# Performance work log

Hardware: AMD Instinct MI355X
Metric: run time of the kernel (lower is better)

The kernel has to match this reference:

```python
import jax, jax.numpy as jnp
import numpy as np

H = 16
D_MODEL = 1024
D_K = D_MODEL // H


def setup_inputs() -> dict:
    key = jax.random.key(0)
    ks = jax.random.split(key, 11)
    B, S = 2, 2048
    scale = 1.0 / np.sqrt(D_MODEL)
    inp = {
        "query": jax.random.normal(ks[0], (B, S, D_MODEL), dtype=jnp.float32),
        "key": jax.random.normal(ks[1], (B, S, D_MODEL), dtype=jnp.float32),
        "value": jax.random.normal(ks[2], (B, S, D_MODEL), dtype=jnp.float32),
        "Wq": jax.random.normal(ks[3], (D_MODEL, D_MODEL), dtype=jnp.float32) * scale,
        "bq": jnp.zeros((D_MODEL,), dtype=jnp.float32),
        "Wk": jax.random.normal(ks[4], (D_MODEL, D_MODEL), dtype=jnp.float32) * scale,
        "bk": jnp.zeros((D_MODEL,), dtype=jnp.float32),
        "Wv": jax.random.normal(ks[5], (D_MODEL, D_MODEL), dtype=jnp.float32) * scale,
        "bv": jnp.zeros((D_MODEL,), dtype=jnp.float32),
        "Wo": jax.random.normal(ks[6], (D_MODEL, D_MODEL), dtype=jnp.float32) * scale,
        "bo": jnp.zeros((D_MODEL,), dtype=jnp.float32),
    }
    return inp


def _mha(query, key, value, Wq, bq, Wk, bk, Wv, bv, Wo, bo):
    B, S, _ = query.shape
    # linear projections (torch nn.Linear: x @ W.T + b)
    q = query @ Wq.T + bq
    k = key @ Wk.T + bk
    v = value @ Wv.T + bv
    # split heads: [B, S, D] -> [B, H, S, d_k]
    q = q.reshape(B, S, H, D_K).transpose(0, 2, 1, 3)
    k = k.reshape(B, S, H, D_K).transpose(0, 2, 1, 3)
    v = v.reshape(B, S, H, D_K).transpose(0, 2, 1, 3)
    # scaled dot-product attention with manual stable softmax
    scores = jnp.einsum("bhqd,bhkd->bhqk", q, k) / jnp.sqrt(jnp.float32(D_K))
    stable = scores - jnp.max(scores, axis=-1, keepdims=True)
    e = jnp.exp(stable)
    attn = e / jnp.sum(e, axis=-1, keepdims=True)
    ctx = jnp.einsum("bhqk,bhkd->bhqd", attn, v)
    # merge heads and final projection
    ctx = ctx.transpose(0, 2, 1, 3).reshape(B, S, H * D_K)
    return ctx @ Wo.T + bo


def reference(query, key, value, Wq, bq, Wk, bk, Wv, bv, Wo, bo):
    return _mha(query, key, value, Wq, bq, Wk, bk, Wv, bv, Wo, bo)
```

## Files before the change

kernel.cpp:

```cpp
#include <hip/hip_runtime.h>


#define S_LEN 2048
#define BATCH 2
#define DM    1024
#define NH    16
#define DKH   64
#define BS    (BATCH * S_LEN)

typedef _Float16 f16x8 __attribute__((ext_vector_type(8)));
typedef _Float16 f16x4 __attribute__((ext_vector_type(4)));
typedef _Float16 f16x2 __attribute__((ext_vector_type(2)));
typedef __fp16   h16x2 __attribute__((ext_vector_type(2)));
typedef float    f32x4 __attribute__((ext_vector_type(4)));
typedef float    f32x16 __attribute__((ext_vector_type(16)));

__device__ __forceinline__ f16x2 pk_f16(float a, float b) {
  h16x2 r = __builtin_amdgcn_cvt_pkrtz(a, b);
  return __builtin_bit_cast(f16x2, r);
}

__device__ __forceinline__ void gld16(const void* g, void* l) {
  __builtin_amdgcn_global_load_lds(
      (const __attribute__((address_space(1))) void*)g,
      (__attribute__((address_space(3))) void*)l, 16, 0, 0);
}

__device__ __forceinline__ float fast_exp2(float x) {
#if __has_builtin(__builtin_amdgcn_exp2f)
  return __builtin_amdgcn_exp2f(x);
#else
  return exp2f(x);
#endif
}

__device__ __forceinline__ int swap23(int x) {
  return (x & ~12) | ((x & 4) << 1) | ((x & 8) >> 1);
}

__device__ __forceinline__ f16x8 cvt8(const float* __restrict__ p) {
  float4 x0 = *(const float4*)p;
  float4 x1 = *(const float4*)(p + 4);
  f16x2 c0 = pk_f16(x0.x, x0.y), c1 = pk_f16(x0.z, x0.w);
  f16x2 c2 = pk_f16(x1.x, x1.y), c3 = pk_f16(x1.z, x1.w);
  f16x8 h;
  h[0] = c0[0]; h[1] = c0[1]; h[2] = c1[0]; h[3] = c1[1];
  h[4] = c2[0]; h[5] = c2[1]; h[6] = c3[0]; h[7] = c3[1];
  return h;
}

template <typename OUT_T, bool VT, bool A32, bool B32>
__device__ __forceinline__ void gemm_core(
    const void* __restrict__ Av, const void* __restrict__ Wv,
    const float* __restrict__ bias, OUT_T* __restrict__ out, float oscale)
{
  const int tid  = threadIdx.x;
  const int l    = tid & 63;
  const int wv   = tid >> 6;
  const int c    = l & 15, quad = l >> 4;
  const int m0   = blockIdx.x * 128, n0 = blockIdx.y * 128;
  const int wm   = wv & 1, wn = wv >> 1;
  __shared__ _Float16 sA[128 * 64];
  __shared__ _Float16 sB[128 * 64];

  const _Float16* gA16[4]; const float* gA32[4];
  const _Float16* gB16[4]; const float* gB32[4];
#pragma unroll
  for (int p = 0; p < 4; ++p) {
    int s = tid + p * 256, r = s >> 3, g = (s & 7) ^ (r & 7);
    if constexpr (A32) gA32[p] = (const float*)Av + (size_t)(m0 + r) * DM + g * 8;
    else               gA16[p] = (const _Float16*)Av + (size_t)(m0 + r) * DM + g * 8;
    if constexpr (B32) gB32[p] = (const float*)Wv + (size_t)(n0 + r) * DM + g * 8;
    else               gB16[p] = (const _Float16*)Wv + (size_t)(n0 + r) * DM + g * 8;
  }
  const int cx = c & 7;

  f32x4 acc[4][4] = {};
  for (int k0 = 0; k0 < DM; k0 += 64) {
    __syncthreads();
    if constexpr (!A32) {
#pragma unroll
      for (int p = 0; p < 4; ++p) gld16(gA16[p] + k0, sA + (tid + p * 256) * 8);
    }
    if constexpr (!B32) {
#pragma unroll
      for (int p = 0; p < 4; ++p) gld16(gB16[p] + k0, sB + (tid + p * 256) * 8);
    }
    if constexpr (A32) {
      f16x8 st[4];
#pragma unroll
      for (int p = 0; p < 4; ++p) st[p] = cvt8(gA32[p] + k0);
#pragma unroll
      for (int p = 0; p < 4; ++p) *(f16x8*)(sA + (tid + p * 256) * 8) = st[p];
    }
    if constexpr (B32) {
      f16x8 st[4];
#pragma unroll
      for (int p = 0; p < 4; ++p) st[p] = cvt8(gB32[p] + k0);
#pragma unroll
      for (int p = 0; p < 4; ++p) *(f16x8*)(sB + (tid + p * 256) * 8) = st[p];
    }
    __syncthreads();
#pragma unroll
    for (int ks = 0; ks < 2; ++ks) {
      f16x8 af[4], bf[4];
#pragma unroll
      for (int i = 0; i < 4; ++i)
        af[i] = *(const f16x8*)&sA[(wm * 64 + i * 16 + c) * 64 + ((ks * 4 + quad) ^ cx) * 8];
#pragma unroll
      for (int j = 0; j < 4; ++j)
        bf[j] = *(const f16x8*)&sB[(wn * 64 + j * 16 + c) * 64 + ((ks * 4 + quad) ^ cx) * 8];
#pragma unroll
      for (int i = 0; i < 4; ++i)
#pragma unroll
        for (int j = 0; j < 4; ++j) {
          if constexpr (VT)
            acc[i][j] = __builtin_amdgcn_mfma_f32_16x16x32_f16(af[i], bf[j], acc[i][j], 0, 0, 0);
          else
            acc[j][i] = __builtin_amdgcn_mfma_f32_16x16x32_f16(bf[j], af[i], acc[j][i], 0, 0, 0);
        }
    }
  }
  if constexpr (VT) {
#pragma unroll
    for (int j = 0; j < 4; ++j) {
      int col = n0 + wn * 64 + j * 16 + c;
      float bb = bias[col];
      int hh = col >> 6, dd = col & 63;
#pragma unroll
      for (int i = 0; i < 4; ++i) {
        int row = m0 + wm * 64 + i * 16 + quad * 4;
        int bb2 = row >> 11, ss = row & (S_LEN - 1);
        _Float16* dst = (_Float16*)out + ((size_t)(bb2 * NH + hh) * DKH + dd) * S_LEN + ss;
        f16x4 v4;
#pragma unroll
        for (int r = 0; r < 4; ++r) v4[r] = (_Float16)((acc[i][j][r] + bb) * oscale);
        *(f16x4*)dst = v4;
      }
    }
  } else {
#pragma unroll
    for (int j = 0; j < 4; ++j) {
      const int nb = n0 + wn * 64 + j * 16 + quad * 4;
      const f32x4 bb = *(const f32x4*)(bias + nb);
#pragma unroll
      for (int i = 0; i < 4; ++i) {
        const int m = m0 + wm * 64 + i * 16 + c;
        if constexpr (__is_same(OUT_T, float)) {
          f32x4 v4;
#pragma unroll
          for (int r = 0; r < 4; ++r) v4[r] = (acc[j][i][r] + bb[r]) * oscale;
          *(f32x4*)((float*)out + (size_t)m * DM + nb) = v4;
        } else {
          f16x4 v4;
#pragma unroll
          for (int r = 0; r < 4; ++r) v4[r] = (_Float16)((acc[j][i][r] + bb[r]) * oscale);
          *(f16x4*)((_Float16*)out + (size_t)m * DM + nb) = v4;
        }
      }
    }
  }
}

#define SC_Q (0.125f * 1.44269504088896340736f)

__global__ __launch_bounds__(256) void proj3(
    const float* __restrict__ xq, const float* __restrict__ xk, const float* __restrict__ xv,
    const float* __restrict__ wqp, const float* __restrict__ wkp, const float* __restrict__ wvp,
    const float* __restrict__ bq, const float* __restrict__ bk, const float* __restrict__ bv,
    _Float16* __restrict__ Q, _Float16* __restrict__ K, _Float16* __restrict__ Vt)
{
  const int z = blockIdx.z;
  if (z == 2) {
    gemm_core<_Float16, true, true, true>(xv, wvp, bv, Vt, 1.0f);
  } else if (z == 0) {
    gemm_core<_Float16, false, true, true>(xq, wqp, bq, Q, SC_Q);
  } else {
    gemm_core<_Float16, false, true, true>(xk, wkp, bk, K, 1.0f);
  }
}

__global__ __launch_bounds__(256) void out_gemm(
    const _Float16* __restrict__ ctx, const float* __restrict__ wo,
    const float* __restrict__ bo, float* __restrict__ out)
{
  gemm_core<float, false, false, true>(ctx, wo, bo, out, 1.0f);
}

__global__ __launch_bounds__(256, 2) void attn(
    const _Float16* __restrict__ Q, const _Float16* __restrict__ K,
    const _Float16* __restrict__ Vt, _Float16* __restrict__ ctx)
{
  const int tid = threadIdx.x;
  const int l   = tid & 63, wv = tid >> 6;
  const int lo5 = l & 31, hf = l >> 5;
  const int wq  = wv >> 1, wk = wv & 1;
  const int bh  = blockIdx.x;
  const int q0  = blockIdx.y * 128;
  const int b   = bh >> 4, hd = bh & 15;
  __shared__ _Float16 sK[2][64 * 64];
  __shared__ _Float16 sV[2][64 * 64];

  f16x8 qf0[4], qf1[4];
  {
    const _Float16* Qg0 = Q + ((size_t)(b * S_LEN + q0 + wq * 64 + lo5)) * DM + hd * DKH + 8 * hf;
    const _Float16* Qg1 = Qg0 + (size_t)32 * DM;
#pragma unroll
    for (int kc = 0; kc < 4; ++kc) { qf0[kc] = *(const f16x8*)(Qg0 + 16 * kc);
                                     qf1[kc] = *(const f16x8*)(Qg1 + 16 * kc); }
  }

  f32x16 o0[2] = {}, o1[2] = {};
  float l0 = 0.f, l1 = 0.f;
  const f16x2 ones = {(_Float16)1.0f, (_Float16)1.0f};

  const _Float16* Kg0 = K + ((size_t)b * S_LEN) * DM + hd * DKH;
  const _Float16* Vg0 = Vt + ((size_t)bh * DKH) * S_LEN;

  const int sa = tid,       ra = sa >> 3, ba = (sa & 7) ^ (ra & 7);
  const int sb = tid + 256, rb = sb >> 3, bb = (sb & 7) ^ (rb & 7);
  const _Float16* gKa = Kg0 + (size_t)swap23(ra) * DM + ba * 8;
  const _Float16* gKb = Kg0 + (size_t)swap23(rb) * DM + bb * 8;
  const _Float16* gVa = Vg0 + (size_t)ra * S_LEN + ba * 8;
  const _Float16* gVb = Vg0 + (size_t)rb * S_LEN + bb * 8;
  const int rx = lo5 & 7;

#define STAGE(t, bf) do {                                   \
    const size_t k0s = (size_t)(t) * 64;                    \
    gld16(gKa + k0s * DM, sK[bf] + sa * 8);                 \
    gld16(gKb + k0s * DM, sK[bf] + sb * 8);                 \
    gld16(gVa + k0s,      sV[bf] + sa * 8);                 \
    gld16(gVb + k0s,      sV[bf] + sb * 8);                 \
  } while (0)

  STAGE(0, 0);
  asm volatile("s_waitcnt vmcnt(0)" ::: "memory");
  __builtin_amdgcn_s_barrier();

  const int NT = S_LEN / 64;
  for (int kt = 0; kt < NT; ++kt) {
    const int cur = kt & 1;
    if (kt + 1 < NT) STAGE(kt + 1, cur ^ 1);

    const _Float16* sKc = sK[cur];
    const _Float16* sVc = sV[cur];

    f32x16 sA0 = {}, sA1 = {};
    __builtin_amdgcn_s_setprio(1);
#pragma unroll
    for (int kc = 0; kc < 4; ++kc) {
      f16x8 kf = *(const f16x8*)&sKc[(32 * wk + lo5) * 64 + ((2 * kc + hf) ^ rx) * 8];
      sA0 = __builtin_amdgcn_mfma_f32_32x32x16_f16(kf, qf0[kc], sA0, 0, 0, 0);
      sA1 = __builtin_amdgcn_mfma_f32_32x32x16_f16(kf, qf1[kc], sA1, 0, 0, 0);
    }
    __builtin_amdgcn_s_setprio(0);

    f16x8 p0[2], p1[2];
#pragma unroll
    for (int half = 0; half < 2; ++half)
#pragma unroll
      for (int j2 = 0; j2 < 4; ++j2) {
        float a0 = fast_exp2(sA0[8 * half + 2 * j2]);
        float a1 = fast_exp2(sA0[8 * half + 2 * j2 + 1]);
        f16x2 pka = pk_f16(a0, a1);
        p0[half][2 * j2]     = pka[0];
        p0[half][2 * j2 + 1] = pka[1];
        l0 = __builtin_amdgcn_fdot2(__builtin_bit_cast(h16x2, pka),
                                    __builtin_bit_cast(h16x2, ones), l0, false);
        float b0 = fast_exp2(sA1[8 * half + 2 * j2]);
        float b1 = fast_exp2(sA1[8 * half + 2 * j2 + 1]);
        f16x2 pkb = pk_f16(b0, b1);
        p1[half][2 * j2]     = pkb[0];
        p1[half][2 * j2 + 1] = pkb[1];
        l1 = __builtin_amdgcn_fdot2(__builtin_bit_cast(h16x2, pkb),
                                    __builtin_bit_cast(h16x2, ones), l1, false);
      }

    __builtin_amdgcn_s_setprio(1);
#pragma unroll
    for (int db = 0; db < 2; ++db)
#pragma unroll
      for (int half = 0; half < 2; ++half) {
        const int kc2 = 2 * wk + half;
        f16x8 vf = *(const f16x8*)&sVc[(32 * db + lo5) * 64 + ((2 * kc2 + hf) ^ rx) * 8];
        o0[db] = __builtin_amdgcn_mfma_f32_32x32x16_f16(p0[half], vf, o0[db], 0, 0, 0);
        o1[db] = __builtin_amdgcn_mfma_f32_32x32x16_f16(p1[half], vf, o1[db], 0, 0, 0);
      }
    __builtin_amdgcn_s_setprio(0);

    if (kt + 1 < NT) {
      asm volatile("s_waitcnt vmcnt(0)" ::: "memory");
      __builtin_amdgcn_s_barrier();
    }
  }
#undef STAGE

  __syncthreads();

  l0 += __shfl_xor(l0, 32);
  l1 += __shfl_xor(l1, 32);
  float* lbuf = (float*)&sV[0][0];
  float* obuf = (float*)&sK[0][0];
  if (hf == 0) {
    lbuf[((wq * 2 + 0) * 2 + wk) * 32 + lo5] = l0;
    lbuf[((wq * 2 + 1) * 2 + wk) * 32 + lo5] = l1;
  }
  __syncthreads();

  float inv0[16], inv1[16];
#pragma unroll
  for (int r = 0; r < 16; ++r) {
    int qq = 8 * (r >> 2) + 4 * hf + (r & 3);
    inv0[r] = 1.0f / (lbuf[((wq * 2 + 0) * 2 + 0) * 32 + qq] +
                      lbuf[((wq * 2 + 0) * 2 + 1) * 32 + qq]);
    inv1[r] = 1.0f / (lbuf[((wq * 2 + 1) * 2 + 0) * 32 + qq] +
                      lbuf[((wq * 2 + 1) * 2 + 1) * 32 + qq]);
  }

  _Float16* Og = ctx + ((size_t)(b * S_LEN + q0 + wq * 64)) * DM + hd * DKH;
#pragma unroll
  for (int db = 0; db < 2; ++db) {
    if (wk == 1) {
#pragma unroll
      for (int r = 0; r < 16; ++r) {
        int qq = 8 * (r >> 2) + 4 * hf + (r & 3);
        obuf[((wq * 2 + 0) * 32 + qq) * 32 + lo5] = o0[db][r];
        obuf[((wq * 2 + 1) * 32 + qq) * 32 + lo5] = o1[db][r];
      }
    }
    __syncthreads();
    if (wk == 0) {
#pragma unroll
      for (int r = 0; r < 16; ++r) {
        int qq = 8 * (r >> 2) + 4 * hf + (r & 3);
        float v0 = o0[db][r] + obuf[((wq * 2 + 0) * 32 + qq) * 32 + lo5];
        float v1 = o1[db][r] + obuf[((wq * 2 + 1) * 32 + qq) * 32 + lo5];
        Og[(size_t)qq * DM + 32 * db + lo5]        = (_Float16)(v0 * inv0[r]);
        Og[(size_t)(32 + qq) * DM + 32 * db + lo5] = (_Float16)(v1 * inv1[r]);
      }
    }
    __syncthreads();
  }
}

extern "C" void kernel_launch(void* const* d_in, const int* in_sizes, int n_in,
                              void* d_out, int out_size, void* d_ws, size_t ws_size,
                              hipStream_t stream)
{
  (void)in_sizes; (void)n_in; (void)out_size; (void)ws_size;
  const float* q  = (const float*)d_in[0];
  const float* k  = (const float*)d_in[1];
  const float* v  = (const float*)d_in[2];
  const float* wq = (const float*)d_in[3];
  const float* bq = (const float*)d_in[4];
  const float* wk = (const float*)d_in[5];
  const float* bk = (const float*)d_in[6];
  const float* wv = (const float*)d_in[7];
  const float* bv = (const float*)d_in[8];
  const float* wo = (const float*)d_in[9];
  const float* bo = (const float*)d_in[10];

  char* ws = (char*)d_ws;
  _Float16* CTX = (_Float16*)(ws);
  _Float16* Qp  = (_Float16*)(ws + (8u  << 20));
  _Float16* Kp  = (_Float16*)(ws + (16u << 20));
  _Float16* VT  = (_Float16*)(ws + (24u << 20));
  float* out = (float*)d_out;

  proj3<<<dim3(32, 8, 3), 256, 0, stream>>>(q, k, v, wq, wk, wv, bq, bk, bv, Qp, Kp, VT);
  attn<<<dim3(32, 16), 256, 0, stream>>>(Qp, Kp, VT, CTX);
  out_gemm<<<dim3(32, 8), 256, 0, stream>>>(CTX, wo, bo, out);
}
```

Before: 242.9 us.

## Pre-convert weights to fp16 and double-buffer projection GEMM loads

Adds a small kernel that converts all four weight matrices to fp16 once per call, so the GEMMs can load weights with direct global-to-LDS copies instead of converting fp32 tiles in every block. The projection GEMM now prefetches the next fp32 activation tile into registers and double-buffers the weight tile in shared memory, overlapping loads with MFMA work. This costs an extra kernel launch and extra LDS plus register pressure in exchange for less per-block conversion traffic and better latency hiding.

```diff
diff --git a/kernel.cpp b/kernel.cpp
--- a/kernel.cpp
+++ b/kernel.cpp
@@ -38,21 +38,34 @@
   return (x & ~12) | ((x & 4) << 1) | ((x & 8) >> 1);
 }
 
-__device__ __forceinline__ f16x8 cvt8(const float* __restrict__ p) {
-  float4 x0 = *(const float4*)p;
-  float4 x1 = *(const float4*)(p + 4);
-  f16x2 c0 = pk_f16(x0.x, x0.y), c1 = pk_f16(x0.z, x0.w);
-  f16x2 c2 = pk_f16(x1.x, x1.y), c3 = pk_f16(x1.z, x1.w);
+__device__ __forceinline__ f16x8 pack8(f32x4 a, f32x4 b) {
+  f16x2 c0 = pk_f16(a[0], a[1]), c1 = pk_f16(a[2], a[3]);
+  f16x2 c2 = pk_f16(b[0], b[1]), c3 = pk_f16(b[2], b[3]);
   f16x8 h;
   h[0] = c0[0]; h[1] = c0[1]; h[2] = c1[0]; h[3] = c1[1];
   h[4] = c2[0]; h[5] = c2[1]; h[6] = c3[0]; h[7] = c3[1];
   return h;
 }
 
-template <typename OUT_T, bool VT, bool A32, bool B32>
-__device__ __forceinline__ void gemm_core(
-    const void* __restrict__ Av, const void* __restrict__ Wv,
-    const float* __restrict__ bias, OUT_T* __restrict__ out, float oscale)
+__global__ __launch_bounds__(256) void cvt_w(
+    const float* __restrict__ wq, const float* __restrict__ wk,
+    const float* __restrict__ wv, const float* __restrict__ wo,
+    _Float16* __restrict__ w16)
+{
+  const int y = blockIdx.y;
+  const float* src = (y == 0) ? wq : (y == 1) ? wk : (y == 2) ? wv : wo;
+  _Float16* dst = w16 + (size_t)y * (DM * DM);
+  int i0 = (blockIdx.x * 256 + threadIdx.x) * 8;
+  f32x4 a = *(const f32x4*)(src + i0);
+  f32x4 b = *(const f32x4*)(src + i0 + 4);
+  *(f16x8*)(dst + i0) = pack8(a, b);
+}
+
+template <typename OUT_T, bool VT>
+__device__ __forceinline__ void gemm_a32(
+    const float* __restrict__ A, const _Float16* __restrict__ W,
+    const float* __restrict__ bias, OUT_T* __restrict__ out, float oscale,
+    _Float16* sA, _Float16* sB)
 {
   const int tid  = threadIdx.x;
   const int l    = tid & 63;
@@ -60,47 +73,49 @@
   const int c    = l & 15, quad = l >> 4;
   const int m0   = blockIdx.x * 128, n0 = blockIdx.y * 128;
   const int wm   = wv & 1, wn = wv >> 1;
-  __shared__ _Float16 sA[128 * 64];
-  __shared__ _Float16 sB[128 * 64];
-
-  const _Float16* gA16[4]; const float* gA32[4];
-  const _Float16* gB16[4]; const float* gB32[4];
+
+  const float* gA[4]; const _Float16* gB[4];
 #pragma unroll
   for (int p = 0; p < 4; ++p) {
     int s = tid + p * 256, r = s >> 3, g = (s & 7) ^ (r & 7);
-    if constexpr (A32) gA32[p] = (const float*)Av + (size_t)(m0 + r) * DM + g * 8;
-    else               gA16[p] = (const _Float16*)Av + (size_t)(m0 + r) * DM + g * 8;
-    if constexpr (B32) gB32[p] = (const float*)Wv + (size_t)(n0 + r) * DM + g * 8;
-    else               gB16[p] = (const _Float16*)Wv + (size_t)(n0 + r) * DM + g * 8;
+    gA[p] = A + (size_t)(m0 + r) * DM + g * 8;
+    gB[p] = W + (size_t)(n0 + r) * DM + g * 8;
   }
   const int cx = c & 7;
 
+  f32x4 pa[8];
+#define LOADA(k0) do {                                        \
+    _Pragma("unroll")                                         \
+    for (int p = 0; p < 4; ++p) {                             \
+      pa[2 * p]     = *(const f32x4*)(gA[p] + (k0));          \
+      pa[2 * p + 1] = *(const f32x4*)(gA[p] + (k0) + 4);      \
+    } } while (0)
+
+  LOADA(0);
+#pragma unroll
+  for (int p = 0; p < 4; ++p) gld16(gB[p], sB + (tid + p * 256) * 8);
+
   f32x4 acc[4][4] = {};
-  for (int k0 = 0; k0 < DM; k0 += 64) {
-    __syncthreads();
-    if constexpr (!A32) {
-#pragma unroll
-      for (int p = 0; p < 4; ++p) gld16(gA16[p] + k0, sA + (tid + p * 256) * 8);
-    }
-    if constexpr (!B32) {
-#pragma unroll
-      for (int p = 0; p < 4; ++p) gld16(gB16[p] + k0, sB + (tid + p * 256) * 8);
-    }
-    if constexpr (A32) {
-      f16x8 st[4];
-#pragma unroll
-      for (int p = 0; p < 4; ++p) st[p] = cvt8(gA32[p] + k0);
-#pragma unroll
-      for (int p = 0; p < 4; ++p) *(f16x8*)(sA + (tid + p * 256) * 8) = st[p];
-    }
-    if constexpr (B32) {
-      f16x8 st[4];
-#pragma unroll
-      for (int p = 0; p < 4; ++p) st[p] = cvt8(gB32[p] + k0);
-#pragma unroll
-      for (int p = 0; p < 4; ++p) *(f16x8*)(sB + (tid + p * 256) * 8) = st[p];
-    }
-    __syncthreads();
+  for (int k0 = 0, kt = 0; k0 < DM; k0 += 64, ++kt) {
+    _Float16* sBc = sB + (kt & 1) * (128 * 64);
+    _Float16* sBn = sB + ((kt & 1) ^ 1) * (128 * 64);
+
+    f16x8 stA[4];
+#pragma unroll
+    for (int p = 0; p < 4; ++p) stA[p] = pack8(pa[2 * p], pa[2 * p + 1]);
+
+    __syncthreads();
+#pragma unroll
+    for (int p = 0; p < 4; ++p) *(f16x8*)(sA + (tid + p * 256) * 8) = stA[p];
+    asm volatile("s_waitcnt vmcnt(0)" ::: "memory");
+    __syncthreads();
+
+    if (k0 + 64 < DM) {
+#pragma unroll
+      for (int p = 0; p < 4; ++p) gld16(gB[p] + k0 + 64, sBn + (tid + p * 256) * 8);
+      LOADA(k0 + 64);
+    }
+
 #pragma unroll
     for (int ks = 0; ks < 2; ++ks) {
       f16x8 af[4], bf[4];
@@ -109,7 +124,7 @@
         af[i] = *(const f16x8*)&sA[(wm * 64 + i * 16 + c) * 64 + ((ks * 4 + quad) ^ cx) * 8];
 #pragma unroll
       for (int j = 0; j < 4; ++j)
-        bf[j] = *(const f16x8*)&sB[(wn * 64 + j * 16 + c) * 64 + ((ks * 4 + quad) ^ cx) * 8];
+        bf[j] = *(const f16x8*)&sBc[(wn * 64 + j * 16 + c) * 64 + ((ks * 4 + quad) ^ cx) * 8];
 #pragma unroll
       for (int i = 0; i < 4; ++i)
 #pragma unroll
@@ -121,6 +136,8 @@
         }
     }
   }
+#undef LOADA
+
   if constexpr (VT) {
 #pragma unroll
     for (int j = 0; j < 4; ++j) {
@@ -146,17 +163,80 @@
 #pragma unroll
       for (int i = 0; i < 4; ++i) {
         const int m = m0 + wm * 64 + i * 16 + c;
-        if constexpr (__is_same(OUT_T, float)) {
-          f32x4 v4;
-#pragma unroll
-          for (int r = 0; r < 4; ++r) v4[r] = (acc[j][i][r] + bb[r]) * oscale;
-          *(f32x4*)((float*)out + (size_t)m * DM + nb) = v4;
-        } else {
-          f16x4 v4;
-#pragma unroll
-          for (int r = 0; r < 4; ++r) v4[r] = (_Float16)((acc[j][i][r] + bb[r]) * oscale);
-          *(f16x4*)((_Float16*)out + (size_t)m * DM + nb) = v4;
-        }
+        f16x4 v4;
+#pragma unroll
+        for (int r = 0; r < 4; ++r) v4[r] = (_Float16)((acc[j][i][r] + bb[r]) * oscale);
+        *(f16x4*)((_Float16*)out + (size_t)m * DM + nb) = v4;
+      }
+    }
+  }
+}
+
+template <typename OUT_T>
+__device__ __forceinline__ void gemm_f16(
+    const _Float16* __restrict__ A, const _Float16* __restrict__ W,
+    const float* __restrict__ bias, OUT_T* __restrict__ out, float oscale,
+    _Float16* sA, _Float16* sB)
+{
+  const int tid  = threadIdx.x;
+  const int l    = tid & 63;
+  const int wv   = tid >> 6;
+  const int c    = l & 15, quad = l >> 4;
+  const int m0   = blockIdx.x * 128, n0 = blockIdx.y * 128;
+  const int wm   = wv & 1, wn = wv >> 1;
+
+  const _Float16* gA[4]; const _Float16* gB[4];
+#pragma unroll
+  for (int p = 0; p < 4; ++p) {
+    int s = tid + p * 256, r = s >> 3, g = (s & 7) ^ (r & 7);
+    gA[p] = A + (size_t)(m0 + r) * DM + g * 8;
+    gB[p] = W + (size_t)(n0 + r) * DM + g * 8;
+  }
+  const int cx = c & 7;
+
+  f32x4 acc[4][4] = {};
+  for (int k0 = 0; k0 < DM; k0 += 64) {
+    __syncthreads();
+#pragma unroll
+    for (int p = 0; p < 4; ++p) {
+      gld16(gA[p] + k0, sA + (tid + p * 256) * 8);
+      gld16(gB[p] + k0, sB + (tid + p * 256) * 8);
+    }
+    asm volatile("s_waitcnt vmcnt(0)" ::: "memory");
+    __syncthreads();
+#pragma unroll
+    for (int ks = 0; ks < 2; ++ks) {
+      f16x8 af[4], bf[4];
+#pragma unroll
+      for (int i = 0; i < 4; ++i)
+        af[i] = *(const f16x8*)&sA[(wm * 64 + i * 16 + c) * 64 + ((ks * 4 + quad) ^ cx) * 8];
+#pragma unroll
+      for (int j = 0; j < 4; ++j)
+        bf[j] = *(const f16x8*)&sB[(wn * 64 + j * 16 + c) * 64 + ((ks * 4 + quad) ^ cx) * 8];
+#pragma unroll
+      for (int i = 0; i < 4; ++i)
+#pragma unroll
+        for (int j = 0; j < 4; ++j)
+          acc[j][i] = __builtin_amdgcn_mfma_f32_16x16x32_f16(bf[j], af[i], acc[j][i], 0, 0, 0);
+    }
+  }
+#pragma unroll
+  for (int j = 0; j < 4; ++j) {
+    const int nb = n0 + wn * 64 + j * 16 + quad * 4;
+    const f32x4 bb = *(const f32x4*)(bias + nb);
+#pragma unroll
+    for (int i = 0; i < 4; ++i) {
+      const int m = m0 + wm * 64 + i * 16 + c;
+      if constexpr (__is_same(OUT_T, float)) {
+        f32x4 v4;
+#pragma unroll
+        for (int r = 0; r < 4; ++r) v4[r] = (acc[j][i][r] + bb[r]) * oscale;
+        *(f32x4*)((float*)out + (size_t)m * DM + nb) = v4;
+      } else {
+        f16x4 v4;
+#pragma unroll
+        for (int r = 0; r < 4; ++r) v4[r] = (_Float16)((acc[j][i][r] + bb[r]) * oscale);
+        *(f16x4*)((_Float16*)out + (size_t)m * DM + nb) = v4;
       }
     }
   }
@@ -166,25 +246,29 @@
 
 __global__ __launch_bounds__(256) void proj3(
     const float* __restrict__ xq, const float* __restrict__ xk, const float* __restrict__ xv,
-    const float* __restrict__ wqp, const float* __restrict__ wkp, const float* __restrict__ wvp,
+    const _Float16* __restrict__ w16,
     const float* __restrict__ bq, const float* __restrict__ bk, const float* __restrict__ bv,
     _Float16* __restrict__ Q, _Float16* __restrict__ K, _Float16* __restrict__ Vt)
 {
+  __shared__ _Float16 smem[3 * 128 * 64];
   const int z = blockIdx.z;
   if (z == 2) {
-    gemm_core<_Float16, true, true, true>(xv, wvp, bv, Vt, 1.0f);
+    gemm_a32<_Float16, true>(xv, w16 + (size_t)2 * DM * DM, bv, Vt, 1.0f,
+                             smem, smem + 128 * 64);
   } else if (z == 0) {
-    gemm_core<_Float16, false, true, true>(xq, wqp, bq, Q, SC_Q);
+    gemm_a32<_Float16, false>(xq, w16, bq, Q, SC_Q, smem, smem + 128 * 64);
   } else {
-    gemm_core<_Float16, false, true, true>(xk, wkp, bk, K, 1.0f);
+    gemm_a32<_Float16, false>(xk, w16 + (size_t)DM * DM, bk, K, 1.0f,
+                              smem, smem + 128 * 64);
   }
 }
 
 __global__ __launch_bounds__(256) void out_gemm(
-    const _Float16* __restrict__ ctx, const float* __restrict__ wo,
+    const _Float16* __restrict__ ctx, const _Float16* __restrict__ wo16,
     const float* __restrict__ bo, float* __restrict__ out)
 {
-  gemm_core<float, false, false, true>(ctx, wo, bo, out, 1.0f);
+  __shared__ _Float16 smem[2 * 128 * 64];
+  gemm_f16<float>(ctx, wo16, bo, out, 1.0f, smem, smem + 128 * 64);
 }
 
 __global__ __launch_bounds__(256, 2) void attn(
@@ -365,9 +449,11 @@
   _Float16* Qp  = (_Float16*)(ws + (8u  << 20));
   _Float16* Kp  = (_Float16*)(ws + (16u << 20));
   _Float16* VT  = (_Float16*)(ws + (24u << 20));
+  _Float16* W16 = (_Float16*)(ws + (32u << 20));
   float* out = (float*)d_out;
 
-  proj3<<<dim3(32, 8, 3), 256, 0, stream>>>(q, k, v, wq, wk, wv, bq, bk, bv, Qp, Kp, VT);
+  cvt_w<<<dim3(512, 4), 256, 0, stream>>>(wq, wk, wv, wo, W16);
+  proj3<<<dim3(32, 8, 3), 256, 0, stream>>>(q, k, v, W16, bq, bk, bv, Qp, Kp, VT);
   attn<<<dim3(32, 16), 256, 0, stream>>>(Qp, Kp, VT, CTX);
-  out_gemm<<<dim3(32, 8), 256, 0, stream>>>(CTX, wo, bo, out);
-}
+  out_gemm<<<dim3(32, 8), 256, 0, stream>>>(CTX, W16 + (size_t)3 * DM * DM, bo, out);
+}
```

Result: faster. 222.9 us (-8.2%).

## Register-prefetch next GEMM tile to overlap global loads with MFMA compute

Applied to the files above, without the earlier changes.

The projection and output GEMMs now load the next K-tile from global memory into registers while the current tile is being computed, instead of loading synchronously between barriers. The fp16 path drops the direct global-to-LDS loads and stages through registers as well. The aim is to hide global memory latency behind the MFMA work. In exchange it uses more registers for the prefetch buffers, which may lower occupancy, and the scheduling now relies on manual barriers and waitcnt.

```diff
diff --git a/kernel.cpp b/kernel.cpp
--- a/kernel.cpp
+++ b/kernel.cpp
@@ -38,11 +38,9 @@
   return (x & ~12) | ((x & 4) << 1) | ((x & 8) >> 1);
 }
 
-__device__ __forceinline__ f16x8 cvt8(const float* __restrict__ p) {
-  float4 x0 = *(const float4*)p;
-  float4 x1 = *(const float4*)(p + 4);
-  f16x2 c0 = pk_f16(x0.x, x0.y), c1 = pk_f16(x0.z, x0.w);
-  f16x2 c2 = pk_f16(x1.x, x1.y), c3 = pk_f16(x1.z, x1.w);
+__device__ __forceinline__ f16x8 pack8(f32x4 a, f32x4 b) {
+  f16x2 c0 = pk_f16(a[0], a[1]), c1 = pk_f16(a[2], a[3]);
+  f16x2 c2 = pk_f16(b[0], b[1]), c3 = pk_f16(b[2], b[3]);
   f16x8 h;
   h[0] = c0[0]; h[1] = c0[1]; h[2] = c1[0]; h[3] = c1[1];
   h[4] = c2[0]; h[5] = c2[1]; h[6] = c3[0]; h[7] = c3[1];
@@ -50,9 +48,10 @@
 }
 
 template <typename OUT_T, bool VT, bool A32, bool B32>
-__device__ __forceinline__ void gemm_core(
+__device__ __forceinline__ void gemm_rs(
     const void* __restrict__ Av, const void* __restrict__ Wv,
-    const float* __restrict__ bias, OUT_T* __restrict__ out, float oscale)
+    const float* __restrict__ bias, OUT_T* __restrict__ out, float oscale,
+    _Float16* sA, _Float16* sB)
 {
   const int tid  = threadIdx.x;
   const int l    = tid & 63;
@@ -60,11 +59,9 @@
   const int c    = l & 15, quad = l >> 4;
   const int m0   = blockIdx.x * 128, n0 = blockIdx.y * 128;
   const int wm   = wv & 1, wn = wv >> 1;
-  __shared__ _Float16 sA[128 * 64];
-  __shared__ _Float16 sB[128 * 64];
-
-  const _Float16* gA16[4]; const float* gA32[4];
-  const _Float16* gB16[4]; const float* gB32[4];
+
+  const float* gA32[4]; const _Float16* gA16[4];
+  const float* gB32[4]; const _Float16* gB16[4];
 #pragma unroll
   for (int p = 0; p < 4; ++p) {
     int s = tid + p * 256, r = s >> 3, g = (s & 7) ^ (r & 7);
@@ -75,32 +72,53 @@
   }
   const int cx = c & 7;
 
+  f32x4 pa[8]; f16x8 pa16[4];
+  f32x4 pb[8]; f16x8 pb16[4];
+
+#define LOADT(k0) do {                                                         \
+    _Pragma("unroll")                                                          \
+    for (int p = 0; p < 4; ++p) {                                              \
+      if constexpr (A32) {                                                     \
+        pa[2 * p]     = *(const f32x4*)(gA32[p] + (k0));                       \
+        pa[2 * p + 1] = *(const f32x4*)(gA32[p] + (k0) + 4);                   \
+      } else {                                                                 \
+        pa16[p] = *(const f16x8*)(gA16[p] + (k0));                             \
+      }                                                                        \
+      if constexpr (B32) {                                                     \
+        pb[2 * p]     = *(const f32x4*)(gB32[p] + (k0));                       \
+        pb[2 * p + 1] = *(const f32x4*)(gB32[p] + (k0) + 4);                   \
+      } else {                                                                 \
+        pb16[p] = *(const f16x8*)(gB16[p] + (k0));                             \
+      }                                                                        \
+    } } while (0)
+
+  LOADT(0);
+
   f32x4 acc[4][4] = {};
   for (int k0 = 0; k0 < DM; k0 += 64) {
-    __syncthreads();
-    if constexpr (!A32) {
-#pragma unroll
-      for (int p = 0; p < 4; ++p) gld16(gA16[p] + k0, sA + (tid + p * 256) * 8);
-    }
-    if constexpr (!B32) {
-#pragma unroll
-      for (int p = 0; p < 4; ++p) gld16(gB16[p] + k0, sB + (tid + p * 256) * 8);
-    }
-    if constexpr (A32) {
-      f16x8 st[4];
-#pragma unroll
-      for (int p = 0; p < 4; ++p) st[p] = cvt8(gA32[p] + k0);
-#pragma unroll
-      for (int p = 0; p < 4; ++p) *(f16x8*)(sA + (tid + p * 256) * 8) = st[p];
-    }
-    if constexpr (B32) {
-      f16x8 st[4];
-#pragma unroll
-      for (int p = 0; p < 4; ++p) st[p] = cvt8(gB32[p] + k0);
-#pragma unroll
-      for (int p = 0; p < 4; ++p) *(f16x8*)(sB + (tid + p * 256) * 8) = st[p];
-    }
-    __syncthreads();
+    f16x8 stA[4], stB[4];
+#pragma unroll
+    for (int p = 0; p < 4; ++p) {
+      if constexpr (A32) stA[p] = pack8(pa[2 * p], pa[2 * p + 1]);
+      else               stA[p] = pa16[p];
+      if constexpr (B32) stB[p] = pack8(pb[2 * p], pb[2 * p + 1]);
+      else               stB[p] = pb16[p];
+    }
+
+    __builtin_amdgcn_sched_barrier(0);
+    __builtin_amdgcn_s_barrier();
+    __builtin_amdgcn_sched_barrier(0);
+#pragma unroll
+    for (int p = 0; p < 4; ++p) {
+      *(f16x8*)(sA + (tid + p * 256) * 8) = stA[p];
+      *(f16x8*)(sB + (tid + p * 256) * 8) = stB[p];
+    }
+    if (k0 + 64 < DM) LOADT(k0 + 64);
+    asm volatile("s_waitcnt lgkmcnt(0)" ::: "memory");
+    __builtin_amdgcn_sched_barrier(0);
+    __builtin_amdgcn_s_barrier();
+    __builtin_amdgcn_sched_barrier(0);
+
 #pragma unroll
     for (int ks = 0; ks < 2; ++ks) {
       f16x8 af[4], bf[4];
@@ -121,6 +139,8 @@
         }
     }
   }
+#undef LOADT
+
   if constexpr (VT) {
 #pragma unroll
     for (int j = 0; j < 4; ++j) {
@@ -170,13 +190,14 @@
     const float* __restrict__ bq, const float* __restrict__ bk, const float* __restrict__ bv,
     _Float16* __restrict__ Q, _Float16* __restrict__ K, _Float16* __restrict__ Vt)
 {
+  __shared__ _Float16 smem[2 * 128 * 64];
   const int z = blockIdx.z;
   if (z == 2) {
-    gemm_core<_Float16, true, true, true>(xv, wvp, bv, Vt, 1.0f);
+    gemm_rs<_Float16, true, true, true>(xv, wvp, bv, Vt, 1.0f, smem, smem + 128 * 64);
   } else if (z == 0) {
-    gemm_core<_Float16, false, true, true>(xq, wqp, bq, Q, SC_Q);
+    gemm_rs<_Float16, false, true, true>(xq, wqp, bq, Q, SC_Q, smem, smem + 128 * 64);
   } else {
-    gemm_core<_Float16, false, true, true>(xk, wkp, bk, K, 1.0f);
+    gemm_rs<_Float16, false, true, true>(xk, wkp, bk, K, 1.0f, smem, smem + 128 * 64);
   }
 }
 
@@ -184,7 +205,8 @@
     const _Float16* __restrict__ ctx, const float* __restrict__ wo,
     const float* __restrict__ bo, float* __restrict__ out)
 {
-  gemm_core<float, false, false, true>(ctx, wo, bo, out, 1.0f);
+  __shared__ _Float16 smem[2 * 128 * 64];
+  gemm_rs<float, false, false, true>(ctx, wo, bo, out, 1.0f, smem, smem + 128 * 64);
 }
 
 __global__ __launch_bounds__(256, 2) void attn(
```

Result: faster. 225.8 us (-7.0%).
